# Kernel optimization log

Hardware: AMD Instinct MI355X
Metric: run time of the kernel (lower is better)

The kernel has to match this reference:

```python
import jax, jax.numpy as jnp
import numpy as np

B, S, D = 2, 2048, 1024
H, A = 16, 64  # num_heads, attention_dim


def setup_inputs() -> dict:
    key = jax.random.key(0)
    ks = jax.random.split(key, 9)
    sd = D ** -0.5
    so = (H * A) ** -0.5
    return {
        "x": jax.random.normal(ks[0], (B, S, D), dtype=jnp.float32),
        "Wq": jax.random.normal(ks[1], (D, H * A), dtype=jnp.float32) * sd,
        "bq": jnp.zeros((H * A,), dtype=jnp.float32),
        "Wk": jax.random.normal(ks[2], (D, H * A), dtype=jnp.float32) * sd,
        "bk": jnp.zeros((H * A,), dtype=jnp.float32),
        "Wv": jax.random.normal(ks[3], (D, H * A), dtype=jnp.float32) * sd,
        "bv": jnp.zeros((H * A,), dtype=jnp.float32),
        "Wo": jax.random.normal(ks[4], (H * A, D), dtype=jnp.float32) * so,
        "bo": jnp.zeros((D,), dtype=jnp.float32),
    }


def reference(x, Wq, bq, Wk, bk, Wv, bv, Wo, bo):
    b, s, _ = x.shape
    # project and split heads: [b, s, H, A]
    q = (x @ Wq + bq).reshape(b, s, H, A)
    k = (x @ Wk + bk).reshape(b, s, H, A)
    v = (x @ Wv + bv).reshape(b, s, H, A)
    # scores [b, H, s, s]
    scores = jnp.einsum("bqhd,bkhd->bhqk", q, k) / jnp.sqrt(jnp.float32(A))
    weights = jax.nn.softmax(scores, axis=-1)
    attended = jnp.einsum("bhqk,bkhd->bqhd", weights, v).reshape(b, s, H * A)
    return attended @ Wo + bo
```

## Files before the change

kernel.cpp:

```cpp
#include <hip/hip_runtime.h>
#include <hip/hip_bf16.h>

typedef __attribute__((ext_vector_type(8))) short bf16x8;
typedef __attribute__((ext_vector_type(4))) float f32x4;

#define LOG2E 1.44269504088896f

extern "C" __device__ float __ocml_native_exp2_f32(float);

__device__ __forceinline__ unsigned short f2bf(float f) {
    union { float f; unsigned int u; } v; v.f = f;
    unsigned int r = v.u + 0x7FFF + ((v.u >> 16) & 1);
    return (unsigned short)(r >> 16);
}

__device__ __forceinline__ unsigned int pk_bf16(float lo, float hi) {
    unsigned int r;
    asm("v_cvt_pk_bf16_f32 %0, %1, %2" : "=v"(r) : "v"(lo), "v"(hi));
    return r;
}

typedef __attribute__((address_space(3))) unsigned int lds_uint;
typedef __attribute__((address_space(1))) const unsigned int glob_uint;
__device__ __forceinline__ void gl2lds16(const void* g, void* l) {
    __builtin_amdgcn_global_load_lds((glob_uint*)g, (lds_uint*)l, 16, 0, 0);
}

__global__ __launch_bounds__(256) void cvt_bf16(const float* __restrict__ in,
                                                unsigned int* __restrict__ out, int n4) {
    int i = blockIdx.x * 256 + threadIdx.x;
    if (i >= n4) return;
    float4 v = ((const float4*)in)[i];
    uint2 o;
    o.x = pk_bf16(v.x, v.y);
    o.y = pk_bf16(v.z, v.w);
    ((uint2*)out)[i] = o;
}

__global__ __launch_bounds__(256) void transpose4_bf16(
    const float* __restrict__ w0, const float* __restrict__ w1,
    const float* __restrict__ w2, const float* __restrict__ w3,
    unsigned short* __restrict__ o0, unsigned short* __restrict__ o1,
    unsigned short* __restrict__ o2, unsigned short* __restrict__ o3) {
    const int z = blockIdx.z;
    const float* in = (z == 0) ? w0 : (z == 1) ? w1 : (z == 2) ? w2 : w3;
    unsigned short* out = (z == 0) ? o0 : (z == 1) ? o1 : (z == 2) ? o2 : o3;
    __shared__ float t[32][33];
    int tx = threadIdx.x & 31, ty = threadIdx.x >> 5;
    int r0 = blockIdx.y * 32, c0 = blockIdx.x * 32;
    for (int i = 0; i < 32; i += 8)
        t[ty + i][tx] = in[(size_t)(r0 + ty + i) * 1024 + c0 + tx];
    __syncthreads();
    for (int i = 0; i < 32; i += 8)
        out[(size_t)(c0 + ty + i) * 1024 + r0 + tx] = f2bf(t[tx][ty + i]);
}

__device__ __forceinline__ void gemm_core(const short* __restrict__ A,
                                          const short* __restrict__ BT,
                                          int K, int bm0, int bn0,
                                          short* As, short* Bs, f32x4 acc[4][4]) {
    const int tid = threadIdx.x;
    const int lane = tid & 63;
    const int w = tid >> 6;
    const int wr0 = (w >> 1) * 64;
    const int wc0 = (w & 1) * 64;
    const int l15 = lane & 15, quad = lane >> 4;
    const int sr = lane >> 2;
    const int slog = (lane & 3) ^ (sr & 3);

    for (int i = 0; i < 4; i++)
        for (int j = 0; j < 4; j++) acc[i][j] = (f32x4)0.f;

    for (int k0 = 0; k0 < K; k0 += 32) {
        for (int i = 0; i < 4; i++) {
            int c = w * 4 + i;
            if (c < 8)
                gl2lds16(A + (size_t)(bm0 + c * 16 + sr) * K + k0 + slog * 8,
                         As + c * 512);
            else
                gl2lds16(BT + (size_t)(bn0 + (c - 8) * 16 + sr) * K + k0 + slog * 8,
                         Bs + (c - 8) * 512);
        }
        __syncthreads();
        const int ph = (quad ^ (l15 & 3)) * 8;
        bf16x8 af[4], bfr[4];
        for (int im = 0; im < 4; im++)
            af[im] = *(const bf16x8*)&As[(wr0 + im * 16 + l15) * 32 + ph];
        for (int in = 0; in < 4; in++)
            bfr[in] = *(const bf16x8*)&Bs[(wc0 + in * 16 + l15) * 32 + ph];
        for (int im = 0; im < 4; im++)
            for (int in = 0; in < 4; in++)
                acc[im][in] = __builtin_amdgcn_mfma_f32_16x16x32_bf16(af[im], bfr[in], acc[im][in], 0, 0, 0);
        __syncthreads();
    }
}

__global__ __launch_bounds__(256) void gemm_qkv(
    const short* __restrict__ xb,
    const short* __restrict__ wqT, const short* __restrict__ wkT, const short* __restrict__ wvT,
    const float* __restrict__ bq, const float* __restrict__ bk, const float* __restrict__ bv,
    unsigned short* __restrict__ qb, unsigned short* __restrict__ kb, unsigned short* __restrict__ vTb) {
    __shared__ short As[4096], Bs[4096];
    const int z = blockIdx.z;
    const short* Amat = (z == 2) ? wvT : xb;
    const short* Bmat = (z == 0) ? wqT : (z == 1) ? wkT : xb;
    const float* bias = (z == 0) ? bq : (z == 1) ? bk : bv;
    const float scl = (z == 0) ? 0.125f * LOG2E : 1.f;
    const int bm0 = (z == 2) ? blockIdx.y * 128 : blockIdx.x * 128;
    const int bn0 = (z == 2) ? blockIdx.x * 128 : blockIdx.y * 128;
    f32x4 acc[4][4];
    gemm_core(Amat, Bmat, 1024, bm0, bn0, As, Bs, acc);
    const int lane = threadIdx.x & 63, w = threadIdx.x >> 6;
    const int wr0 = (w >> 1) * 64, wc0 = (w & 1) * 64, l15 = lane & 15, quad = lane >> 4;
    if (z == 2) {
        for (int im = 0; im < 4; im++)
            for (int in = 0; in < 4; in++)
                for (int r = 0; r < 4; r++) {
                    int rowa = bm0 + wr0 + im * 16 + quad * 4 + r;
                    int colg = bn0 + wc0 + in * 16 + l15;
                    unsigned short ov = f2bf(acc[im][in][r] + bias[rowa]);
                    int b = colg >> 11, s = colg & 2047;
                    vTb[(size_t)b * 2097152 + (size_t)rowa * 2048 + s] = ov;
                }
    } else {
        for (int im = 0; im < 4; im++)
            for (int in = 0; in < 4; in++)
                for (int r = 0; r < 4; r++) {
                    int rowg = bm0 + wr0 + im * 16 + quad * 4 + r;
                    int colg = bn0 + wc0 + in * 16 + l15;
                    unsigned short ov = f2bf((acc[im][in][r] + bias[colg]) * scl);
                    int b = rowg >> 11, s = rowg & 2047;
                    int h = colg >> 6, a = colg & 63;
                    int bh = b * 16 + h;
                    if (z == 0) qb[((size_t)bh * 2048 + s) * 64 + a] = ov;
                    else        kb[((size_t)bh * 2048 + s) * 64 + a] = ov;
                }
    }
}

__global__ __launch_bounds__(256) void gemm_out(
    const short* __restrict__ att, const short* __restrict__ woT,
    const float* __restrict__ bo, float* __restrict__ out) {
    __shared__ short As[4096], Bs[4096];
    const int bm0 = blockIdx.x * 128, bn0 = blockIdx.y * 128;
    f32x4 acc[4][4];
    gemm_core(att, woT, 1024, bm0, bn0, As, Bs, acc);
    const int lane = threadIdx.x & 63, w = threadIdx.x >> 6;
    const int wr0 = (w >> 1) * 64, wc0 = (w & 1) * 64, l15 = lane & 15, quad = lane >> 4;
    for (int im = 0; im < 4; im++)
        for (int in = 0; in < 4; in++)
            for (int r = 0; r < 4; r++) {
                int rowg = bm0 + wr0 + im * 16 + quad * 4 + r;
                int colg = bn0 + wc0 + in * 16 + l15;
                out[(size_t)rowg * 1024 + colg] = acc[im][in][r] + bo[colg];
            }
}

__global__ __launch_bounds__(512, 4) void flash_attn(
    const unsigned short* __restrict__ qb, const unsigned short* __restrict__ kb,
    const unsigned short* __restrict__ vTb, unsigned short* __restrict__ att) {
    __shared__ short QP[9216];
    __shared__ short Ks[2][4096];
    __shared__ short Vs[2][4096];
    const int tid = threadIdx.x, lane = tid & 63, w = tid >> 6;
    const int l15 = lane & 15, quad = lane >> 4;
    const int q0 = blockIdx.x * 128;
    const int bh = blockIdx.y;
    const size_t qkbase = (size_t)bh * 2048 * 64;
    const size_t vbase = (size_t)bh * 64 * 2048;
    const int sr = lane >> 3;
    const int slog = (lane & 7) ^ sr;
    const int l7 = l15 & 7;

    for (int i = 0; i < 4; i++) {
        int c = w * 4 + i;
        if (c < 16)
            gl2lds16(qb + qkbase + (size_t)(q0 + c * 8 + sr) * 64 + slog * 8, QP + c * 512);
        else if (c < 24)
            gl2lds16(kb + qkbase + (size_t)((c - 16) * 8 + sr) * 64 + slog * 8,
                     Ks[0] + (c - 16) * 512);
        else
            gl2lds16(vTb + vbase + (size_t)((c - 24) * 8 + sr) * 2048 + slog * 8,
                     Vs[0] + (c - 24) * 512);
    }
    __syncthreads();

    const int wq0 = w * 16;
    const int c0 = (quad ^ l7) * 8, c1 = c0 ^ 32;
    const int fb = l15 * 64;
    bf16x8 aq0 = *(const bf16x8*)&QP[(wq0 + l15) * 64 + c0];
    bf16x8 aq1 = *(const bf16x8*)&QP[(wq0 + l15) * 64 + c1];
    __syncthreads();

    f32x4 o[4];
    for (int dt = 0; dt < 4; dt++) o[dt] = (f32x4)0.f;
    f32x4 ls = (f32x4)0.f;

    short* Pw = QP + w * 16 * 72;
    short* Pst = Pw + l15 * 72 + quad * 4;
    const short* Prd = Pw + l15 * 72 + quad * 8;

    const unsigned short* sgp;
    int sgstep; int sg2;
    const int slo = (w & 3) * 1024;
    if (w < 4) {
        sgp = kb + qkbase + (size_t)(64 + w * 16 + sr) * 64 + slog * 8;
        sgstep = 4096; sg2 = 512;
    } else {
        sgp = vTb + vbase + (size_t)((w - 4) * 16 + sr) * 2048 + 64 + slog * 8;
        sgstep = 64; sg2 = 16384;
    }
    short* sb0 = (w < 4 ? Ks[0] : Vs[0]) + slo;
    short* sb1 = (w < 4 ? Ks[1] : Vs[1]) + slo;

    auto step = [&](const short* Kb, const short* Vb, bool stage,
                    const unsigned short* sg, short* sd) {
        if (stage) {
            gl2lds16(sg, sd);
            gl2lds16(sg + sg2, sd + 512);
        }
        f32x4 sc[4];
#pragma unroll
        for (int t = 0; t < 4; t++) {
            bf16x8 ak = *(const bf16x8*)(Kb + fb + c0 + t * 1024);
            sc[t] = __builtin_amdgcn_mfma_f32_16x16x32_bf16(ak, aq0, (f32x4)0.f, 0, 0, 0);
        }
#pragma unroll
        for (int t = 0; t < 4; t++) {
            bf16x8 ak = *(const bf16x8*)(Kb + fb + c1 + t * 1024);
            sc[t] = __builtin_amdgcn_mfma_f32_16x16x32_bf16(ak, aq1, sc[t], 0, 0, 0);
        }
#pragma unroll
        for (int t = 0; t < 4; t++) {
#pragma unroll
            for (int r = 0; r < 4; r++) sc[t][r] = __ocml_native_exp2_f32(sc[t][r]);
            ls += sc[t];
            uint2 pk;
            pk.x = pk_bf16(sc[t][0], sc[t][1]);
            pk.y = pk_bf16(sc[t][2], sc[t][3]);
            *(uint2*)(Pst + t * 16) = pk;
        }
#pragma unroll
        for (int t2 = 0; t2 < 2; t2++) {
            bf16x8 bp = *(const bf16x8*)(Prd + t2 * 32);
            const int cc = t2 ? c1 : c0;
#pragma unroll
            for (int dt = 0; dt < 4; dt++) {
                bf16x8 av = *(const bf16x8*)(Vb + fb + cc + dt * 1024);
                o[dt] = __builtin_amdgcn_mfma_f32_16x16x32_bf16(av, bp, o[dt], 0, 0, 0);
            }
        }
        __syncthreads();
    };

    for (int kv0 = 0; kv0 < 2048; kv0 += 128) {
        step(Ks[0], Vs[0], true, sgp, sb1);
        sgp += sgstep;
        step(Ks[1], Vs[1], kv0 + 128 < 2048, sgp, sb0);
        sgp += sgstep;
    }

    const int b = bh >> 4, h = bh & 15;
    float l = (ls[0] + ls[1]) + (ls[2] + ls[3]);
    l += __shfl_xor(l, 16);
    l += __shfl_xor(l, 32);
    float inv = 1.f / l;
    int s = q0 + wq0 + l15;
    for (int dt = 0; dt < 4; dt++) {
        uint2 pk;
        pk.x = pk_bf16(o[dt][0] * inv, o[dt][1] * inv);
        pk.y = pk_bf16(o[dt][2] * inv, o[dt][3] * inv);
        int col = h * 64 + dt * 16 + quad * 4;
        *(uint2*)&att[((size_t)b * 2048 + s) * 1024 + col] = pk;
    }
}

extern "C" void kernel_launch(void* const* d_in, const int* in_sizes, int n_in,
                              void* d_out, int out_size, void* d_ws, size_t ws_size,
                              hipStream_t stream) {
    const float* x  = (const float*)d_in[0];
    const float* Wq = (const float*)d_in[1];
    const float* bq = (const float*)d_in[2];
    const float* Wk = (const float*)d_in[3];
    const float* bk = (const float*)d_in[4];
    const float* Wv = (const float*)d_in[5];
    const float* bv = (const float*)d_in[6];
    const float* Wo = (const float*)d_in[7];
    const float* bo = (const float*)d_in[8];
    float* out = (float*)d_out;

    short* ws  = (short*)d_ws;
    short* xb  = ws;
    short* wqT = ws + 4 * 1024 * 1024;
    short* wkT = wqT + 1024 * 1024;
    short* wvT = wkT + 1024 * 1024;
    short* woT = wvT + 1024 * 1024;
    short* qb  = woT + 1024 * 1024;
    short* kb  = qb + 4 * 1024 * 1024;
    short* vTb = kb + 4 * 1024 * 1024;
    short* att = vTb + 4 * 1024 * 1024;

    cvt_bf16<<<4096, 256, 0, stream>>>(x, (unsigned int*)xb, 1024 * 1024);
    transpose4_bf16<<<dim3(32, 32, 4), 256, 0, stream>>>(
        Wq, Wk, Wv, Wo,
        (unsigned short*)wqT, (unsigned short*)wkT,
        (unsigned short*)wvT, (unsigned short*)woT);
    gemm_qkv<<<dim3(32, 8, 3), 256, 0, stream>>>(xb, wqT, wkT, wvT, bq, bk, bv,
                                                 (unsigned short*)qb, (unsigned short*)kb,
                                                 (unsigned short*)vTb);
    flash_attn<<<dim3(16, 32), 512, 0, stream>>>((const unsigned short*)qb,
                                                 (const unsigned short*)kb,
                                                 (const unsigned short*)vTb,
                                                 (unsigned short*)att);
    gemm_out<<<dim3(32, 8), 256, 0, stream>>>(att, woT, bo, out);
}
```

Measured before the change: 210.0 us.

## Deepen KV pipeline to four buffers and pass P via lane permutes

Replaces the double-buffered K/V staging with a four-stage ring that keeps three tiles in flight, using vmcnt-based waits and raw barriers instead of a full __syncthreads per step. The P matrix is now re-laid out in registers with permlane32/permlane16 swaps rather than written to and read back from LDS. s_setprio is also raised around the MFMA sections. Together these target global-load latency and the LDS round trip for P. The cost is more LDS use per block (Q plus four K and four V buffers), which may limit occupancy, and the hand-counted vmcnt values must match the issued loads exactly.

```diff
diff --git a/kernel.cpp b/kernel.cpp
--- a/kernel.cpp
+++ b/kernel.cpp
@@ -159,9 +159,9 @@
 __global__ __launch_bounds__(512, 4) void flash_attn(
     const unsigned short* __restrict__ qb, const unsigned short* __restrict__ kb,
     const unsigned short* __restrict__ vTb, unsigned short* __restrict__ att) {
-    __shared__ short QP[9216];
-    __shared__ short Ks[2][4096];
-    __shared__ short Vs[2][4096];
+    __shared__ short Qs[8192];
+    __shared__ short Ks[4][4096];
+    __shared__ short Vs[4][4096];
     const int tid = threadIdx.x, lane = tid & 63, w = tid >> 6;
     const int l15 = lane & 15, quad = lane >> 4;
     const int q0 = blockIdx.x * 128;
@@ -172,54 +172,49 @@
     const int slog = (lane & 7) ^ sr;
     const int l7 = l15 & 7;
 
-    for (int i = 0; i < 4; i++) {
-        int c = w * 4 + i;
-        if (c < 16)
-            gl2lds16(qb + qkbase + (size_t)(q0 + c * 8 + sr) * 64 + slog * 8, QP + c * 512);
-        else if (c < 24)
-            gl2lds16(kb + qkbase + (size_t)((c - 16) * 8 + sr) * 64 + slog * 8,
-                     Ks[0] + (c - 16) * 512);
-        else
-            gl2lds16(vTb + vbase + (size_t)((c - 24) * 8 + sr) * 2048 + slog * 8,
-                     Vs[0] + (c - 24) * 512);
-    }
-    __syncthreads();
+    const unsigned short* sgp;
+    int sgstep, sg2;
+    short* sgb;
+    if (w < 4) {
+        sgp = kb + qkbase + (size_t)(w * 16 + sr) * 64 + slog * 8;
+        sgstep = 4096; sg2 = 512;
+        sgb = &Ks[0][0] + w * 1024;
+    } else {
+        sgp = vTb + vbase + (size_t)((w - 4) * 16 + sr) * 2048 + slog * 8;
+        sgstep = 64; sg2 = 16384;
+        sgb = &Vs[0][0] + (w - 4) * 1024;
+    }
+    auto stage_tile = [&](int buf) {
+        short* sd = sgb + buf * 4096;
+        gl2lds16(sgp, sd);
+        gl2lds16(sgp + sg2, sd + 512);
+        sgp += sgstep;
+    };
+
+    for (int i = 0; i < 2; i++) {
+        int c = w * 2 + i;
+        gl2lds16(qb + qkbase + (size_t)(q0 + c * 8 + sr) * 64 + slog * 8, Qs + c * 512);
+    }
+    stage_tile(0); stage_tile(1); stage_tile(2);
+    asm volatile("s_waitcnt vmcnt(4)" ::: "memory");
+    __builtin_amdgcn_s_barrier();
+    asm volatile("" ::: "memory");
 
     const int wq0 = w * 16;
     const int c0 = (quad ^ l7) * 8, c1 = c0 ^ 32;
     const int fb = l15 * 64;
-    bf16x8 aq0 = *(const bf16x8*)&QP[(wq0 + l15) * 64 + c0];
-    bf16x8 aq1 = *(const bf16x8*)&QP[(wq0 + l15) * 64 + c1];
-    __syncthreads();
+    bf16x8 aq0 = *(const bf16x8*)&Qs[(wq0 + l15) * 64 + c0];
+    bf16x8 aq1 = *(const bf16x8*)&Qs[(wq0 + l15) * 64 + c1];
 
     f32x4 o[4];
     for (int dt = 0; dt < 4; dt++) o[dt] = (f32x4)0.f;
     f32x4 ls = (f32x4)0.f;
 
-    short* Pw = QP + w * 16 * 72;
-    short* Pst = Pw + l15 * 72 + quad * 4;
-    const short* Prd = Pw + l15 * 72 + quad * 8;
-
-    const unsigned short* sgp;
-    int sgstep; int sg2;
-    const int slo = (w & 3) * 1024;
-    if (w < 4) {
-        sgp = kb + qkbase + (size_t)(64 + w * 16 + sr) * 64 + slog * 8;
-        sgstep = 4096; sg2 = 512;
-    } else {
-        sgp = vTb + vbase + (size_t)((w - 4) * 16 + sr) * 2048 + 64 + slog * 8;
-        sgstep = 64; sg2 = 16384;
-    }
-    short* sb0 = (w < 4 ? Ks[0] : Vs[0]) + slo;
-    short* sb1 = (w < 4 ? Ks[1] : Vs[1]) + slo;
-
-    auto step = [&](const short* Kb, const short* Vb, bool stage,
-                    const unsigned short* sg, short* sd) {
-        if (stage) {
-            gl2lds16(sg, sd);
-            gl2lds16(sg + sg2, sd + 512);
-        }
+    auto attn_step = [&](int buf) {
+        const short* Kb = &Ks[0][0] + buf * 4096;
+        const short* Vb = &Vs[0][0] + buf * 4096;
         f32x4 sc[4];
+        __builtin_amdgcn_s_setprio(1);
 #pragma unroll
         for (int t = 0; t < 4; t++) {
             bf16x8 ak = *(const bf16x8*)(Kb + fb + c0 + t * 1024);
@@ -230,35 +225,57 @@
             bf16x8 ak = *(const bf16x8*)(Kb + fb + c1 + t * 1024);
             sc[t] = __builtin_amdgcn_mfma_f32_16x16x32_bf16(ak, aq1, sc[t], 0, 0, 0);
         }
+        __builtin_amdgcn_s_setprio(0);
 #pragma unroll
         for (int t = 0; t < 4; t++) {
 #pragma unroll
             for (int r = 0; r < 4; r++) sc[t][r] = __ocml_native_exp2_f32(sc[t][r]);
             ls += sc[t];
-            uint2 pk;
-            pk.x = pk_bf16(sc[t][0], sc[t][1]);
-            pk.y = pk_bf16(sc[t][2], sc[t][3]);
-            *(uint2*)(Pst + t * 16) = pk;
-        }
+        }
+        bf16x8 bp[2];
 #pragma unroll
         for (int t2 = 0; t2 < 2; t2++) {
-            bf16x8 bp = *(const bf16x8*)(Prd + t2 * 32);
+            unsigned pa = pk_bf16(sc[2 * t2][0], sc[2 * t2][1]);
+            unsigned pb = pk_bf16(sc[2 * t2][2], sc[2 * t2][3]);
+            unsigned pc = pk_bf16(sc[2 * t2 + 1][0], sc[2 * t2 + 1][1]);
+            unsigned pd = pk_bf16(sc[2 * t2 + 1][2], sc[2 * t2 + 1][3]);
+            asm("v_permlane32_swap_b32 %0, %1" : "+v"(pa), "+v"(pc));
+            asm("v_permlane32_swap_b32 %0, %1" : "+v"(pb), "+v"(pd));
+            asm("v_permlane16_swap_b32 %0, %1" : "+v"(pa), "+v"(pc));
+            asm("v_permlane16_swap_b32 %0, %1" : "+v"(pb), "+v"(pd));
+            union { unsigned u[4]; bf16x8 v; } cvt;
+            cvt.u[0] = pa; cvt.u[1] = pb; cvt.u[2] = pc; cvt.u[3] = pd;
+            bp[t2] = cvt.v;
+        }
+        __builtin_amdgcn_s_setprio(1);
+#pragma unroll
+        for (int t2 = 0; t2 < 2; t2++) {
             const int cc = t2 ? c1 : c0;
 #pragma unroll
             for (int dt = 0; dt < 4; dt++) {
                 bf16x8 av = *(const bf16x8*)(Vb + fb + cc + dt * 1024);
-                o[dt] = __builtin_amdgcn_mfma_f32_16x16x32_bf16(av, bp, o[dt], 0, 0, 0);
+                o[dt] = __builtin_amdgcn_mfma_f32_16x16x32_bf16(av, bp[t2], o[dt], 0, 0, 0);
             }
         }
-        __syncthreads();
+        __builtin_amdgcn_s_setprio(0);
     };
 
-    for (int kv0 = 0; kv0 < 2048; kv0 += 128) {
-        step(Ks[0], Vs[0], true, sgp, sb1);
-        sgp += sgstep;
-        step(Ks[1], Vs[1], kv0 + 128 < 2048, sgp, sb0);
-        sgp += sgstep;
-    }
+    for (int t = 0; t < 29; t++) {
+        stage_tile((t + 3) & 3);
+        attn_step(t & 3);
+        asm volatile("s_waitcnt vmcnt(4)" ::: "memory");
+        __builtin_amdgcn_s_barrier();
+        asm volatile("" ::: "memory");
+    }
+    attn_step(1);
+    asm volatile("s_waitcnt vmcnt(2)" ::: "memory");
+    __builtin_amdgcn_s_barrier();
+    asm volatile("" ::: "memory");
+    attn_step(2);
+    asm volatile("s_waitcnt vmcnt(0)" ::: "memory");
+    __builtin_amdgcn_s_barrier();
+    asm volatile("" ::: "memory");
+    attn_step(3);
 
     const int b = bh >> 4, h = bh & 15;
     float l = (ls[0] + ls[1]) + (ls[2] + ls[3]);
```

Result: faster. 200.3 us (-4.6%).
